# Kernel tuning notes

Measured on AMD Instinct MI355X. Metric: run time of the kernel, lower is better.

## Reference

```python
import jax, jax.numpy as jnp
import numpy as np

B, T, D, V, L = 16, 1024, 512, 5000, 128
BLANK = 0
NEG = -1e30  # log-space 'zero' (avoid inf for stability)


def setup_inputs() -> dict:
    key = jax.random.key(0)
    k1, k2, k3, k4, k5 = jax.random.split(key, 5)
    hs_pad = jax.random.normal(k1, (B, T, D), jnp.float32)
    W = jax.random.normal(k2, (D, V), jnp.float32) * 0.02
    b = jnp.zeros((V,), jnp.float32)
    hlens = jax.random.randint(k3, (B,), T // 2, T + 1)          # frame lengths
    ys_lens = jax.random.randint(k4, (B,), 64, L + 1)             # label lengths
    ys_pad = jax.random.randint(k5, (B, L), 1, V)                 # labels, no blank
    return {"hs_pad": hs_pad, "hlens": hlens, "ys_pad": ys_pad,
            "ys_lens": ys_lens, "W": W, "b": b}


def _lse3(a, b, c):
    m = jnp.maximum(jnp.maximum(a, b), c)
    m = jnp.maximum(m, NEG)
    return m + jnp.log(jnp.exp(a - m) + jnp.exp(b - m) + jnp.exp(c - m))


def _ctc_loss(logp, hlens, ys_pad, ys_lens):
    # logp: (B, T, V) log-probabilities
    Bb, Tt, _ = logp.shape
    Ll = ys_pad.shape[1]
    S = 2 * Ll + 1
    # extended label sequence: blank, y1, blank, y2, ..., blank  -> (B, S)
    ext = jnp.full((Bb, S), BLANK, ys_pad.dtype).at[:, 1::2].set(ys_pad)
    # gather log-probs of extended labels: (B, T, S)
    lp_ext = jnp.take_along_axis(
        logp, jnp.broadcast_to(ext[:, None, :], (Bb, Tt, S)), axis=2)
    # skip transition from s-2 allowed iff ext[s] != blank and ext[s] != ext[s-2]
    ext_m2 = jnp.pad(ext[:, :-2], ((0, 0), (2, 0)), constant_values=-1)
    allow = (ext != BLANK) & (ext != ext_m2)  # (B, S)

    alpha0 = (jnp.full((Bb, S), NEG, logp.dtype)
              .at[:, 0].set(lp_ext[:, 0, 0])
              .at[:, 1].set(lp_ext[:, 0, 1]))

    def step(alpha, xs):
        lp_t, t = xs
        a1 = alpha
        a2 = jnp.pad(alpha[:, :-1], ((0, 0), (1, 0)), constant_values=NEG)
        a3 = jnp.where(allow,
                       jnp.pad(alpha[:, :-2], ((0, 0), (2, 0)), constant_values=NEG),
                       NEG)
        new = _lse3(a1, a2, a3) + lp_t
        keep = (t < hlens)[:, None]  # freeze alpha past each sequence length
        return jnp.where(keep, new, alpha), None

    lp_seq = jnp.swapaxes(lp_ext, 0, 1)  # (T, B, S)
    ts = jnp.arange(1, Tt)
    alpha, _ = jax.lax.scan(step, alpha0, (lp_seq[1:], ts))

    idx1 = 2 * ys_lens                 # final blank
    idx2 = jnp.maximum(idx1 - 1, 0)    # final label
    a_end = jnp.take_along_axis(alpha, jnp.stack([idx1, idx2], axis=1), axis=1)
    ll = jax.scipy.special.logsumexp(a_end, axis=1)  # (B,)
    loss = -ll
    loss = jnp.where(jnp.isfinite(loss) & (loss < 1e29), loss, 0.0)  # zero_infinity
    # reduction='sum', then normalize by total token count (normalize_length=True)
    return jnp.sum(loss) / jnp.sum(ys_lens).astype(logp.dtype)


def reference(hs_pad, hlens, ys_pad, ys_lens, W, b):
    logits = hs_pad @ W + b                      # (B, T, V), dropout_rate=0
    logp = jax.nn.log_softmax(logits, axis=2)    # same math as transpose->log_softmax
    return _ctc_loss(logp, hlens, ys_pad, ys_lens)
```

## Files before the change

kernel.cpp:

```cpp
#include <hip/hip_runtime.h>
#include <hip/hip_bf16.h>
#include <math.h>

#define B_   16
#define T_   1024
#define D_   512
#define V_   5000
#define VP_  5120
#define L_   128
#define S_   257
#define J_   129
#define JP_  160
#define M_   (B_*T_)
#define NT_  40
#define NEGF (-1e30f)
#define LOG2E_F 1.4426950408889634f

typedef __attribute__((ext_vector_type(8))) short short8;
typedef __attribute__((ext_vector_type(4))) float float4v;

__device__ inline void load_lds_16(const void* g, void* l) {
    __builtin_amdgcn_global_load_lds(
        (const __attribute__((address_space(1))) unsigned int*)g,
        (__attribute__((address_space(3))) unsigned int*)l, 16, 0, 0);
}

__device__ inline unsigned short f2bf(float f) {
    union { float f; unsigned int u; } x; x.f = f;
    unsigned int r = x.u + 0x7FFFu + ((x.u >> 16) & 1u);
    return (unsigned short)(r >> 16);
}

__device__ inline float wave_shr1_f32(float v) {
    return __int_as_float(__builtin_amdgcn_update_dpp(
        0, __float_as_int(v), 0x138, 0xF, 0xF, true));
}
__device__ inline int wave_shr1_i32(int v) {
    return __builtin_amdgcn_update_dpp(0, v, 0x138, 0xF, 0xF, true);
}

__global__ __launch_bounds__(256) void k_convert_hs(
    const float* __restrict__ hs, unsigned short* __restrict__ Ah)
{
    size_t base = ((size_t)blockIdx.x * 256 + threadIdx.x) * 8;
    float4 a = *(const float4*)&hs[base];
    float4 b = *(const float4*)&hs[base + 4];
    short8 o;
    o[0] = (short)f2bf(a.x); o[1] = (short)f2bf(a.y);
    o[2] = (short)f2bf(a.z); o[3] = (short)f2bf(a.w);
    o[4] = (short)f2bf(b.x); o[5] = (short)f2bf(b.y);
    o[6] = (short)f2bf(b.z); o[7] = (short)f2bf(b.w);
    *(short8*)&Ah[base] = o;
}

__global__ __launch_bounds__(256) void k_transpose_w(
    const float* __restrict__ W, unsigned short* __restrict__ Wt)
{
    __shared__ float tile[32][33];
    int v0 = blockIdx.x * 32, k0 = blockIdx.y * 32;
    int tx = threadIdx.x, ty = threadIdx.y;
#pragma unroll
    for (int r = 0; r < 4; r++) {
        int kk = r * 8 + ty;
        float val = 0.f;
        if (v0 + tx < V_) val = W[(size_t)(k0 + kk) * V_ + v0 + tx];
        tile[kk][tx] = val;
    }
    __syncthreads();
#pragma unroll
    for (int r = 0; r < 4; r++) {
        int vloc = r * 8 + ty;
        Wt[(size_t)(v0 + vloc) * D_ + k0 + tx] = f2bf(tile[tx][vloc]);
    }
}

__global__ __launch_bounds__(512) void k_gemm_lse_mfma(
    const unsigned short* __restrict__ Ah,
    const unsigned short* __restrict__ Wt,
    const float* __restrict__ bias,
    float* __restrict__ part_s)
{
    __shared__ unsigned short As[256 * 32];
    __shared__ unsigned short Bs[128 * 32];
    __shared__ float sm_s[2][256];

    const int bx = blockIdx.x;
    const int by = blockIdx.y;
    const int tid = threadIdx.x;
    const int rowBase = bx * 256, colBase = by * 128;
    const int lane = tid & 63, wv = tid >> 6;
    const int wi = wv >> 1, wj = wv & 1;
    const int g = lane >> 4, lo = lane & 15;
    const int cs = g ^ (lo & 3);

    float4v acc[4][4];
#pragma unroll
    for (int i = 0; i < 4; i++)
#pragma unroll
        for (int j = 0; j < 4; j++) acc[i][j] = (float4v){0.f, 0.f, 0.f, 0.f};

    for (int it = 0; it < 16; it++) {
        const int k0 = it * 32;
        __syncthreads();
#pragma unroll
        for (int l = 0; l < 3; l++) {
            int slot = tid + l * 512;
            if (slot < 1024) {
                int r = slot >> 2, q = slot & 3;
                int qs = q ^ (r & 3);
                load_lds_16(&Ah[(size_t)(rowBase + r) * D_ + k0 + qs * 8],
                            &As[r * 32 + q * 8]);
            } else {
                int s = slot - 1024;
                int r = s >> 2, q = s & 3;
                int qs = q ^ (r & 3);
                load_lds_16(&Wt[(size_t)(colBase + r) * D_ + k0 + qs * 8],
                            &Bs[r * 32 + q * 8]);
            }
        }
        __syncthreads();

        short8 a[4], b[4];
#pragma unroll
        for (int i = 0; i < 4; i++)
            a[i] = *(const short8*)&As[(wi * 64 + i * 16 + lo) * 32 + cs * 8];
#pragma unroll
        for (int j = 0; j < 4; j++)
            b[j] = *(const short8*)&Bs[(wj * 64 + j * 16 + lo) * 32 + cs * 8];
#pragma unroll
        for (int i = 0; i < 4; i++)
#pragma unroll
            for (int j = 0; j < 4; j++)
                acc[i][j] = __builtin_amdgcn_mfma_f32_16x16x32_bf16(
                    a[i], b[j], acc[i][j], 0, 0, 0);
    }

    float bj[4]; bool vj[4];
#pragma unroll
    for (int j = 0; j < 4; j++) {
        int col = colBase + wj * 64 + j * 16 + lo;
        vj[j] = (col < V_);
        bj[j] = vj[j] ? bias[col] : 0.f;
    }
#pragma unroll
    for (int i = 0; i < 4; i++) {
#pragma unroll
        for (int r = 0; r < 4; r++) {
            float s = 0.f;
#pragma unroll
            for (int j = 0; j < 4; j++)
                if (vj[j]) s += __expf(acc[i][j][r] + bj[j]);
#pragma unroll
            for (int off = 1; off < 16; off <<= 1)
                s += __shfl_xor(s, off, 16);
            if (lo == 0)
                sm_s[wj][wi * 64 + i * 16 + g * 4 + r] = s;
        }
    }
    __syncthreads();
    if (tid < 256)
        part_s[(size_t)(rowBase + tid) * NT_ + by] = sm_s[0][tid] + sm_s[1][tid];
}

__global__ __launch_bounds__(64) void k_gather_wb(
    const unsigned short* __restrict__ Wt,
    const float* __restrict__ bias,
    const int* __restrict__ ys,
    unsigned short* __restrict__ Wgb,
    float* __restrict__ bgb)
{
    int b = blockIdx.x, j = blockIdx.y;
    int lab = 0;
    if (j >= 1 && j <= L_) lab = ys[b * L_ + (j - 1)];
    else if (j > L_) lab = VP_ - 1;
    const unsigned short* src = &Wt[(size_t)lab * D_];
    unsigned short* dst = &Wgb[((size_t)b * JP_ + j) * D_];
    int t = threadIdx.x;
    *(short8*)&dst[t * 8] = *(const short8*)&src[t * 8];
    if (t == 0) bgb[b * JP_ + j] = (j <= L_) ? bias[lab] : 0.f;
}

__global__ __launch_bounds__(256) void k_label_mfma(
    const unsigned short* __restrict__ Ah,
    const unsigned short* __restrict__ Wgb,
    const float* __restrict__ bgb,
    const float* __restrict__ part_s,
    float* __restrict__ ll,
    float* __restrict__ lb2)
{
    __shared__ unsigned short As[64 * 32];
    __shared__ unsigned short Bs[JP_ * 32];
    __shared__ float outs[64][JP_ + 1];

    const int b = blockIdx.x, t0 = blockIdx.y * 64;
    const int tid = threadIdx.x;
    const int lane = tid & 63, w = tid >> 6;
    const int g = lane >> 4, lo = lane & 15;

    const unsigned short* Ab = Ah  + ((size_t)b * T_ + t0) * D_;
    const unsigned short* Bb = Wgb + (size_t)b * JP_ * D_;

    float4v acc[10];
#pragma unroll
    for (int j = 0; j < 10; j++) acc[j] = (float4v){0.f, 0.f, 0.f, 0.f};

    for (int it = 0; it < 16; it++) {
        const int k0 = it * 32;
        __syncthreads();
        {
            int r = tid >> 2, q = tid & 3;
            load_lds_16(&Ab[(size_t)r * D_ + k0 + q * 8], &As[r * 32 + q * 8]);
        }
        for (int s = tid; s < 640; s += 256) {
            int r = s >> 2, q = s & 3;
            load_lds_16(&Bb[(size_t)r * D_ + k0 + q * 8], &Bs[r * 32 + q * 8]);
        }
        __syncthreads();

        short8 a = *(const short8*)&As[(w * 16 + lo) * 32 + g * 8];
#pragma unroll
        for (int j = 0; j < 10; j++) {
            short8 bf = *(const short8*)&Bs[(j * 16 + lo) * 32 + g * 8];
            acc[j] = __builtin_amdgcn_mfma_f32_16x16x32_bf16(a, bf, acc[j], 0, 0, 0);
        }
    }

#pragma unroll
    for (int j = 0; j < 10; j++) {
        float bv = bgb[b * JP_ + j * 16 + lo];
#pragma unroll
        for (int r = 0; r < 4; r++)
            outs[w * 16 + g * 4 + r][j * 16 + lo] = acc[j][r] + bv;
    }
    __syncthreads();
    for (int idx = tid; idx < 64 * J_; idx += 256) {
        int r = idx / J_, j = idx - r * J_;
        float l0 = outs[r][0];
        float v  = outs[r][j];
        ll[((size_t)b * T_ + t0 + r) * J_ + j] = (j == 0) ? 1.f : __expf(v - l0);
    }
    if (tid < 64) {
        size_t row = (size_t)b * T_ + t0 + tid;
        const float* ps = &part_s[row * NT_];
        float s = 0.f;
#pragma unroll
        for (int i = 0; i < NT_; i++) s += ps[i];
        lb2[row] = (outs[tid][0] - __logf(s)) * LOG2E_F;
    }
}

#define CH_   32
#define CHB_  (CH_ * J_ * 4)
#define NLD_  ((CHB_ + 1023) / 1024)

__global__ __launch_bounds__(64, 1) void k_ctc_alpha(
    const float* __restrict__ Pr,
    const float* __restrict__ lb2,
    const int* __restrict__ hlens,
    const int* __restrict__ ys,
    const int* __restrict__ ys_lens,
    float* __restrict__ loss_b)
{
    __shared__ float llds[2][NLD_ * 256];
    __shared__ float fin_m[S_];
    __shared__ int   fin_e[S_];
    const int b = blockIdx.x;
    const int l = threadIdx.x;
    const int hl = hlens[b];
    const float* prb = Pr  + (size_t)b * T_ * J_;
    const float* lbb = lb2 + (size_t)b * T_;

    double acc = 0.0;
    for (int tt = l; tt < hl; tt += 64) acc += (double)lbb[tt];
#pragma unroll
    for (int off = 32; off > 0; off >>= 1)
        acc += __shfl_xor(acc, off, 64);

    float u1f = 0.f, u3f;
    {
        const int* yb = ys + b * L_;
        if (l >= 1) u1f = (yb[2 * l] != yb[2 * l - 1]) ? 1.f : 0.f;
        u3f = (yb[2 * l + 1] != yb[2 * l]) ? 1.f : 0.f;
    }
    const int c1 = 2 * l + 1;

    float a0 = (l == 0) ? 1.f : 0.f;
    float a1 = (l == 0) ? prb[1] : 0.f;
    float a2 = 0.f, a3 = 0.f, a4 = 0.f;
    int   E  = 0;
    float fl   = (l == 0) ? 0.f : 1.f;
    float u1fl = u1f * fl;

#define RENORM() do {                                                         \
        float mx_ = fmaxf(fmaxf(fmaxf(a0, a1), fmaxf(a2, a3)), a4);           \
        unsigned long long act_ = __ballot(mx_ > 0.f);                        \
        int La_ = 63 - __builtin_clzll(act_);           \
        if (mx_ > 0.f) {                                                      \
            int e_ = (int)((__float_as_uint(mx_) >> 23) & 255u) - 127;        \
            a0 = ldexpf(a0, -e_); a1 = ldexpf(a1, -e_); a2 = ldexpf(a2, -e_); \
            a3 = ldexpf(a3, -e_); a4 = ldexpf(a4, -e_);                       \
            E += e_;                                                          \
        }                                                                     \
        int Ea_ = __shfl(E, La_, 64);                                         \
        if (!(mx_ > 0.f)) E = Ea_;                   \
        int Ep_ = wave_shr1_i32(E);                                           \
        int dE_ = Ep_ - E;                                                    \
        dE_ = dE_ > 126 ? 126 : (dE_ < -126 ? -126 : dE_);                    \
        fl = (l == 0) ? 0.f : ldexpf(1.f, dE_);                               \
        u1fl = u1f * fl;                                                      \
    } while (0)

#define STEP_P(p1_, p3_) do {                                                 \
        float prev_ = wave_shr1_f32(a3);                                      \
        float n0_ = fmaf(prev_, fl, a0);                                      \
        float n1_ = fmaf(prev_, u1fl, a0 + a1) * (p1_);                       \
        float n2_ = a2 + a1;                                                  \
        float n3_ = fmaf(a1, u3f, a3 + a2) * (p3_);                           \
        float n4_ = a4 + a3;                                                  \
        a0 = n0_; a1 = n1_; a2 = n2_; a3 = n3_; a4 = n4_;                     \
    } while (0)

    {
        const char* src = (const char*)prb;
        char* dst = (char*)&llds[0][0];
#pragma unroll
        for (int k = 0; k < NLD_; k++)
            load_lds_16(src + (size_t)k * 1024 + (size_t)l * 16, dst + k * 1024);
    }

    const int nch = (hl + CH_ - 1) / CH_;
    int t = 1;
    for (int c = 0; c < nch; c++) {
        asm volatile("s_waitcnt vmcnt(0)" ::: "memory");
        __builtin_amdgcn_sched_barrier(0);
        if (c + 1 < nch) {
            const char* src = (const char*)(prb + (size_t)(c + 1) * CH_ * J_);
            char* dst = (char*)&llds[(c + 1) & 1][0];
#pragma unroll
            for (int k = 0; k < NLD_; k++)
                load_lds_16(src + (size_t)k * 1024 + (size_t)l * 16, dst + k * 1024);
        }
        const float* lbuf = &llds[c & 1][0];
        const int cbase = c * CH_;
        const int tcap = (hl < cbase + CH_) ? hl : cbase + CH_;
        const int tmid = (tcap < cbase + 16) ? tcap : cbase + 16;
#pragma unroll
        for (int half = 0; half < 2; half++) {
            const int tlim = (half == 0) ? tmid : tcap;
            while (t + 8 <= tlim) {
                float pv1[8], pv3[8];
#pragma unroll
                for (int i = 0; i < 8; i++) {
                    int r = t + i - cbase;
                    pv1[i] = lbuf[r * J_ + c1];
                    pv3[i] = lbuf[r * J_ + c1 + 1];
                }
#pragma unroll
                for (int i = 0; i < 8; i++) STEP_P(pv1[i], pv3[i]);
                t += 8;
            }
            while (t < tlim) {
                int r = t - cbase;
                float p1 = lbuf[r * J_ + c1];
                float p3 = lbuf[r * J_ + c1 + 1];
                STEP_P(p1, p3);
                t++;
            }
            RENORM();
        }
    }

    fin_m[4 * l + 0] = a0; fin_m[4 * l + 1] = a1;
    fin_m[4 * l + 2] = a2; fin_m[4 * l + 3] = a3;
    fin_e[4 * l + 0] = E;  fin_e[4 * l + 1] = E;
    fin_e[4 * l + 2] = E;  fin_e[4 * l + 3] = E;
    if (l == 63) { fin_m[256] = a4; fin_e[256] = E; }
    __syncthreads();

    if (l == 0) {
        int yl = ys_lens[b];
        int i1 = 2 * yl;
        int i2 = (i1 > 0) ? i1 - 1 : 0;
        int Ea = fin_e[i1], Eb = fin_e[i2];
        int Em = Ea > Eb ? Ea : Eb;
        int da = Ea - Em, db = Eb - Em;
        da = da < -126 ? -126 : da;  db = db < -126 ? -126 : db;
        float v = ldexpf(fin_m[i1], da) + ldexpf(fin_m[i2], db);
        float lg = __log2f(v) + (float)Em;
        double lln = ((double)lg + acc) * 0.6931471805599453;
        float loss = -(float)lln;
        if (!isfinite(loss) || loss >= 1e29f) loss = 0.f;
        loss_b[b] = loss;
    }
#undef RENORM
#undef STEP_P
}

__global__ void k_final(const float* __restrict__ loss_b,
                        const int* __restrict__ ys_lens,
                        float* __restrict__ out)
{
    int t = threadIdx.x;
    float v = (t < B_) ? loss_b[t] : 0.f;
    int   n = (t < B_) ? ys_lens[t] : 0;
    for (int off = 32; off > 0; off >>= 1) {
        v += __shfl_down(v, off, 64);
        n += __shfl_down(n, off, 64);
    }
    if (t == 0) out[0] = v / (float)n;
}

extern "C" void kernel_launch(void* const* d_in, const int* in_sizes, int n_in,
                              void* d_out, int out_size, void* d_ws, size_t ws_size,
                              hipStream_t stream)
{
    const float* hs      = (const float*)d_in[0];
    const int*   hlens   = (const int*)  d_in[1];
    const int*   ys      = (const int*)  d_in[2];
    const int*   ys_lens = (const int*)  d_in[3];
    const float* W       = (const float*)d_in[4];
    const float* bias    = (const float*)d_in[5];
    float* out = (float*)d_out;

    float* ws = (float*)d_ws;
    float* part_s = ws;
    unsigned short* Wgb = (unsigned short*)(part_s + (size_t)M_ * NT_);
    float* bgb    = (float*)(Wgb + (size_t)B_ * JP_ * D_);
    float* llab   = bgb    + (size_t)B_ * JP_;
    float* loss_b = llab   + (size_t)B_ * T_ * J_;
    float* lb2    = loss_b + 16;
    unsigned short* Ah = (unsigned short*)(lb2 + M_);
    unsigned short* Wt = Ah + (size_t)M_ * D_;

    k_convert_hs<<<(M_ * D_) / (256 * 8), 256, 0, stream>>>(hs, Ah);
    k_transpose_w<<<dim3(VP_ / 32, D_ / 32), dim3(32, 8), 0, stream>>>(W, Wt);
    k_gemm_lse_mfma<<<dim3(M_ / 256, NT_), 512, 0, stream>>>(Ah, Wt, bias, part_s);
    k_gather_wb<<<dim3(B_, JP_), 64, 0, stream>>>(Wt, bias, ys, Wgb, bgb);
    k_label_mfma<<<dim3(B_, T_ / 64), 256, 0, stream>>>(Ah, Wgb, bgb, part_s, llab, lb2);
    k_ctc_alpha<<<B_, 64, 0, stream>>>(llab, lb2, hlens, ys, ys_lens, loss_b);
    k_final<<<1, 64, 0, stream>>>(loss_b, ys_lens, out);
}
```

Baseline: 263.0 us.

## Double-buffer GEMM LDS tiles and pack CTC alpha waves into two blocks

The GEMM's K loop now uses double-buffered LDS tiles, prefetching the next K slice while MFMAs run on the current one, with one barrier per iteration instead of two. The CTC alpha kernel packs 8 sequences per 512-thread block (2 blocks) instead of 16 single-wave blocks. It also shrinks the per-wave LDS prefetch chunk from 32 to 4 timesteps, renormalises every 16 steps, and reads final alphas via cross-lane shuffles instead of shared memory. Smaller chunks mean more frequent vmcnt waits on the serial recurrence. Putting 8 waves on one CU may also slow the latency-bound alpha scan.

```diff
diff --git a/kernel.cpp b/kernel.cpp
--- a/kernel.cpp
+++ b/kernel.cpp
@@ -80,8 +80,8 @@
     const float* __restrict__ bias,
     float* __restrict__ part_s)
 {
-    __shared__ unsigned short As[256 * 32];
-    __shared__ unsigned short Bs[128 * 32];
+    __shared__ unsigned short As[2][256 * 32];
+    __shared__ unsigned short Bs[2][128 * 32];
     __shared__ float sm_s[2][256];
 
     const int bx = blockIdx.x;
@@ -99,41 +99,48 @@
 #pragma unroll
         for (int j = 0; j < 4; j++) acc[i][j] = (float4v){0.f, 0.f, 0.f, 0.f};
 
+#define STAGE(buf, it) do {                                                   \
+        const int k0_ = (it) * 32;                                            \
+        _Pragma("unroll")                                                     \
+        for (int l_ = 0; l_ < 3; l_++) {                                      \
+            int slot_ = tid + l_ * 512;                                       \
+            if (slot_ < 1024) {                                               \
+                int r_ = slot_ >> 2, q_ = slot_ & 3;                          \
+                int qs_ = q_ ^ (r_ & 3);                                      \
+                load_lds_16(&Ah[(size_t)(rowBase + r_) * D_ + k0_ + qs_ * 8], \
+                            &As[buf][r_ * 32 + q_ * 8]);                      \
+            } else {                                                          \
+                int s_ = slot_ - 1024;                                        \
+                int r_ = s_ >> 2, q_ = s_ & 3;                                \
+                int qs_ = q_ ^ (r_ & 3);                                      \
+                load_lds_16(&Wt[(size_t)(colBase + r_) * D_ + k0_ + qs_ * 8], \
+                            &Bs[buf][r_ * 32 + q_ * 8]);                      \
+            }                                                                 \
+        }                                                                     \
+    } while (0)
+
+    STAGE(0, 0);
+    __syncthreads();
+    int cur = 0;
     for (int it = 0; it < 16; it++) {
-        const int k0 = it * 32;
-        __syncthreads();
-#pragma unroll
-        for (int l = 0; l < 3; l++) {
-            int slot = tid + l * 512;
-            if (slot < 1024) {
-                int r = slot >> 2, q = slot & 3;
-                int qs = q ^ (r & 3);
-                load_lds_16(&Ah[(size_t)(rowBase + r) * D_ + k0 + qs * 8],
-                            &As[r * 32 + q * 8]);
-            } else {
-                int s = slot - 1024;
-                int r = s >> 2, q = s & 3;
-                int qs = q ^ (r & 3);
-                load_lds_16(&Wt[(size_t)(colBase + r) * D_ + k0 + qs * 8],
-                            &Bs[r * 32 + q * 8]);
-            }
-        }
-        __syncthreads();
-
+        if (it < 15) STAGE(cur ^ 1, it + 1);
         short8 a[4], b[4];
 #pragma unroll
         for (int i = 0; i < 4; i++)
-            a[i] = *(const short8*)&As[(wi * 64 + i * 16 + lo) * 32 + cs * 8];
+            a[i] = *(const short8*)&As[cur][(wi * 64 + i * 16 + lo) * 32 + cs * 8];
 #pragma unroll
         for (int j = 0; j < 4; j++)
-            b[j] = *(const short8*)&Bs[(wj * 64 + j * 16 + lo) * 32 + cs * 8];
+            b[j] = *(const short8*)&Bs[cur][(wj * 64 + j * 16 + lo) * 32 + cs * 8];
 #pragma unroll
         for (int i = 0; i < 4; i++)
 #pragma unroll
             for (int j = 0; j < 4; j++)
                 acc[i][j] = __builtin_amdgcn_mfma_f32_16x16x32_bf16(
                     a[i], b[j], acc[i][j], 0, 0, 0);
-    }
+        __syncthreads();
+        cur ^= 1;
+    }
+#undef STAGE
 
     float bj[4]; bool vj[4];
 #pragma unroll
@@ -249,11 +256,10 @@
     }
 }
 
-#define CH_   32
-#define CHB_  (CH_ * J_ * 4)
-#define NLD_  ((CHB_ + 1023) / 1024)
-
-__global__ __launch_bounds__(64, 1) void k_ctc_alpha(
+#define CH_   4
+#define NLD_  3
+
+__global__ __launch_bounds__(512, 1) void k_ctc_alpha(
     const float* __restrict__ Pr,
     const float* __restrict__ lb2,
     const int* __restrict__ hlens,
@@ -261,11 +267,10 @@
     const int* __restrict__ ys_lens,
     float* __restrict__ loss_b)
 {
-    __shared__ float llds[2][NLD_ * 256];
-    __shared__ float fin_m[S_];
-    __shared__ int   fin_e[S_];
-    const int b = blockIdx.x;
-    const int l = threadIdx.x;
+    __shared__ float llds[8][2][NLD_ * 256];
+    const int w = threadIdx.x >> 6;
+    const int l = threadIdx.x & 63;
+    const int b = blockIdx.x * 8 + w;
     const int hl = hlens[b];
     const float* prb = Pr  + (size_t)b * T_ * J_;
     const float* lbb = lb2 + (size_t)b * T_;
@@ -322,70 +327,57 @@
 
     {
         const char* src = (const char*)prb;
-        char* dst = (char*)&llds[0][0];
+        char* dst = (char*)&llds[w][0][0];
 #pragma unroll
         for (int k = 0; k < NLD_; k++)
             load_lds_16(src + (size_t)k * 1024 + (size_t)l * 16, dst + k * 1024);
     }
 
     const int nch = (hl + CH_ - 1) / CH_;
-    int t = 1;
     for (int c = 0; c < nch; c++) {
         asm volatile("s_waitcnt vmcnt(0)" ::: "memory");
         __builtin_amdgcn_sched_barrier(0);
         if (c + 1 < nch) {
             const char* src = (const char*)(prb + (size_t)(c + 1) * CH_ * J_);
-            char* dst = (char*)&llds[(c + 1) & 1][0];
+            char* dst = (char*)&llds[w][(c + 1) & 1][0];
 #pragma unroll
             for (int k = 0; k < NLD_; k++)
                 load_lds_16(src + (size_t)k * 1024 + (size_t)l * 16, dst + k * 1024);
         }
-        const float* lbuf = &llds[c & 1][0];
+        const float* lbuf = &llds[w][c & 1][0];
         const int cbase = c * CH_;
+        const int tt0 = (c == 0) ? 1 : cbase;
         const int tcap = (hl < cbase + CH_) ? hl : cbase + CH_;
-        const int tmid = (tcap < cbase + 16) ? tcap : cbase + 16;
-#pragma unroll
-        for (int half = 0; half < 2; half++) {
-            const int tlim = (half == 0) ? tmid : tcap;
-            while (t + 8 <= tlim) {
-                float pv1[8], pv3[8];
-#pragma unroll
-                for (int i = 0; i < 8; i++) {
-                    int r = t + i - cbase;
-                    pv1[i] = lbuf[r * J_ + c1];
-                    pv3[i] = lbuf[r * J_ + c1 + 1];
-                }
-#pragma unroll
-                for (int i = 0; i < 8; i++) STEP_P(pv1[i], pv3[i]);
-                t += 8;
-            }
-            while (t < tlim) {
-                int r = t - cbase;
+#pragma unroll
+        for (int r = 0; r < CH_; r++) {
+            int tcur = cbase + r;
+            if (tcur >= tt0 && tcur < tcap) {
                 float p1 = lbuf[r * J_ + c1];
                 float p3 = lbuf[r * J_ + c1 + 1];
                 STEP_P(p1, p3);
-                t++;
             }
-            RENORM();
-        }
-    }
-
-    fin_m[4 * l + 0] = a0; fin_m[4 * l + 1] = a1;
-    fin_m[4 * l + 2] = a2; fin_m[4 * l + 3] = a3;
-    fin_e[4 * l + 0] = E;  fin_e[4 * l + 1] = E;
-    fin_e[4 * l + 2] = E;  fin_e[4 * l + 3] = E;
-    if (l == 63) { fin_m[256] = a4; fin_e[256] = E; }
-    __syncthreads();
+        }
+        if ((c & 3) == 3) RENORM();
+    }
+
+    int yl = ys_lens[b];
+    int i1 = 2 * yl, i2 = i1 - 1;
+    int ln1 = (i1 >= 256) ? 63 : (i1 >> 2);
+    int sl1 = (i1 >= 256) ? 4  : (i1 & 3);
+    float cand1 = (sl1 == 0) ? a0 : (sl1 == 1) ? a1 : (sl1 == 2) ? a2
+                : (sl1 == 3) ? a3 : a4;
+    float m1 = __shfl(cand1, ln1, 64);
+    int   E1 = __shfl(E, ln1, 64);
+    int ln2 = i2 >> 2, sl2 = i2 & 3;
+    float cand2 = (sl2 == 0) ? a0 : (sl2 == 1) ? a1 : (sl2 == 2) ? a2 : a3;
+    float m2 = __shfl(cand2, ln2, 64);
+    int   E2 = __shfl(E, ln2, 64);
 
     if (l == 0) {
-        int yl = ys_lens[b];
-        int i1 = 2 * yl;
-        int i2 = (i1 > 0) ? i1 - 1 : 0;
-        int Ea = fin_e[i1], Eb = fin_e[i2];
-        int Em = Ea > Eb ? Ea : Eb;
-        int da = Ea - Em, db = Eb - Em;
-        da = da < -126 ? -126 : da;  db = db < -126 ? -126 : db;
-        float v = ldexpf(fin_m[i1], da) + ldexpf(fin_m[i2], db);
+        int Em = E1 > E2 ? E1 : E2;
+        int d1 = E1 - Em, d2 = E2 - Em;
+        d1 = d1 < -126 ? -126 : d1;  d2 = d2 < -126 ? -126 : d2;
+        float v = ldexpf(m1, d1) + ldexpf(m2, d2);
         float lg = __log2f(v) + (float)Em;
         double lln = ((double)lg + acc) * 0.6931471805599453;
         float loss = -(float)lln;
@@ -437,6 +429,6 @@
     k_gemm_lse_mfma<<<dim3(M_ / 256, NT_), 512, 0, stream>>>(Ah, Wt, bias, part_s);
     k_gather_wb<<<dim3(B_, JP_), 64, 0, stream>>>(Wt, bias, ys, Wgb, bgb);
     k_label_mfma<<<dim3(B_, T_ / 64), 256, 0, stream>>>(Ah, Wgb, bgb, part_s, llab, lb2);
-    k_ctc_alpha<<<B_, 64, 0, stream>>>(llab, lb2, hlens, ys, ys_lens, loss_b);
+    k_ctc_alpha<<<2, 512, 0, stream>>>(llab, lb2, hlens, ys, ys_lens, loss_b);
     k_final<<<1, 64, 0, stream>>>(loss_b, ys_lens, out);
 }
```

Result: slower. 353.9 us (+34.6%).
